# Kernel tuning notes

Measured on AMD Instinct MI355X. Metric: run time of the kernel, lower is better.

Reference implementation:

```python
import jax, jax.numpy as jnp
import numpy as np

N_OSC = 50
N_PER = 40
DT = 0.01
STEPS = 100
# one-link torque limb physical constants (reconstructed)
M_G_LC = 1.0   # m*g*lc gravity torque coefficient
B_DAMP = 0.1   # viscous damping
I_INERTIA = 1.0


def setup_inputs() -> dict:
    key = jax.random.key(0)
    ks = jax.random.split(key, 16)
    B = 8192
    x = jax.random.normal(ks[0], (B, 2), dtype=jnp.float32)
    fc1_w = jax.random.normal(ks[1], (128, 2), dtype=jnp.float32) * 0.5
    fc1_b = jax.random.normal(ks[2], (128,), dtype=jnp.float32) * 0.1
    fc2_w = jax.random.normal(ks[3], (128, 128), dtype=jnp.float32) * 0.08
    fc2_b = jax.random.normal(ks[4], (128,), dtype=jnp.float32) * 0.1
    fc3_w = jax.random.normal(ks[5], (N_OSC * 2, 128), dtype=jnp.float32) * 0.08
    fc3_b = jax.random.normal(ks[6], (N_OSC * 2,), dtype=jnp.float32) * 0.1
    fcd_w = jax.random.normal(ks[7], (1, 128), dtype=jnp.float32) * 0.001  # weight/100
    fcd_b = jnp.zeros((1,), dtype=jnp.float32)                            # bias*0
    enc = jax.random.normal(ks[8], (N_OSC, N_PER, 2), dtype=jnp.float32)
    obias = jax.random.normal(ks[9], (N_OSC, N_PER), dtype=jnp.float32)
    dec = jax.random.normal(ks[10], (N_OSC, 2, N_PER), dtype=jnp.float32) * 0.05
    fc4_w = jax.random.normal(ks[11], (1, N_OSC * N_PER), dtype=jnp.float32) * 1e-4  # weight/10000
    fc4_b = jnp.zeros((1,), dtype=jnp.float32)                                       # bias*0
    return {"x": x, "fc1_w": fc1_w, "fc1_b": fc1_b, "fc2_w": fc2_w, "fc2_b": fc2_b,
            "fc3_w": fc3_w, "fc3_b": fc3_b, "fcd_w": fcd_w, "fcd_b": fcd_b,
            "enc": enc, "obias": obias, "dec": dec, "fc4_w": fc4_w, "fc4_b": fc4_b}


def reference(x, fc1_w, fc1_b, fc2_w, fc2_b, fc3_w, fc3_b, fcd_w, fcd_b,
              enc, obias, dec, fc4_w, fc4_b):
    B = x.shape[0]
    h = jax.nn.relu(x @ fc1_w.T + fc1_b)            # (B,128)
    direct = h @ fcd_w.T + fcd_b                    # (B,1)
    h2 = jax.nn.relu(h @ fc2_w.T + fc2_b)           # (B,128)
    x3 = h2 @ fc3_w.T + fc3_b                       # (B, 2*N_OSC)
    o0 = x3.reshape(B, N_OSC, 2).transpose(1, 0, 2)  # (N_OSC,B,2), xi = x[:, 2j:2j+2]
    l0 = jnp.concatenate([x[:, :1], jnp.zeros((B, 1), dtype=x.dtype)], axis=1)  # (B,2)

    def step(carry, _):
        o, l = carry
        # NEF oscillator activities: relu(state @ encoders^T + bias), vectorized over oscillators
        a = jax.nn.relu(jnp.einsum('obd,ond->obn', o, enc) + obias[:, None, :])  # (N_OSC,B,N_PER)
        o_deriv = jnp.einsum('odn,obn->obd', dec, a)                             # (N_OSC,B,2)
        o = o + DT * o_deriv
        acts = a.transpose(1, 0, 2).reshape(B, N_OSC * N_PER)                    # (B,2000)
        torque = (acts @ fc4_w.T + fc4_b + direct)[:, 0]                         # (B,)
        theta, omega = l[:, 0], l[:, 1]
        alpha = (torque - M_G_LC * jnp.sin(theta) - B_DAMP * omega) / I_INERTIA
        l = l + DT * jnp.stack([omega, alpha], axis=1)
        return (o, l), (l, torque)

    _, (l_states, torques) = jax.lax.scan(step, (o0, l0), None, length=STEPS)
    return l_states, torques  # (STEPS,B,2), (STEPS,B)
```

## Files before the change

### kernel.cpp

```cpp
#include <hip/hip_runtime.h>

#define N_OSC 50
#define N_PER 40
#define DT 0.01f
#define STEPS 100
#define BATCH 8192

typedef float v2f __attribute__((ext_vector_type(2)));

static __device__ __forceinline__ v2f fma2(v2f a, v2f b, v2f c) {
    return __builtin_elementwise_fma(a, b, c);
}

#define WS_PC     0
#define WS_DIRECT 12288
#define WS_O0     20480
#define WS_TORQ   839680

__global__ __launch_bounds__(256) void prep_mlp_kernel(
    const float* __restrict__ x,
    const float* __restrict__ fc1_w, const float* __restrict__ fc1_b,
    const float* __restrict__ fc2_w, const float* __restrict__ fc2_b,
    const float* __restrict__ fc3_w, const float* __restrict__ fc3_b,
    const float* __restrict__ fcd_w, const float* __restrict__ fcd_b,
    const float* __restrict__ enc, const float* __restrict__ obias,
    const float* __restrict__ dec, const float* __restrict__ fc4_w,
    float* __restrict__ pc, float* __restrict__ torq,
    float* __restrict__ o0out, float* __restrict__ directout) {
    __shared__ float hs[16 * 132];
    __shared__ float h2s[16 * 132];
    int blk = blockIdx.x;
    int tid = threadIdx.x;

    if (blk < 800) {
        int idx = blk * 256 + tid;
        ((float4*)torq)[idx] = make_float4(0.f, 0.f, 0.f, 0.f);
        if (idx < N_OSC * N_PER) {
            int o = idx / N_PER, n = idx - o * N_PER;
            int c = n >> 1, h = n & 1;
            float* base = pc + o * 240;
            base[4 * c + h]           = enc[o * 80 + 2 * n + 0];
            base[4 * c + 2 + h]       = enc[o * 80 + 2 * n + 1];
            base[80 + 4 * c + h]      = dec[o * 80 + n];
            base[80 + 4 * c + 2 + h]  = dec[o * 80 + 40 + n];
            base[160 + 2 * c + h]     = fc4_w[o * 40 + n];
            base[200 + 2 * c + h]     = obias[o * 40 + n];
        }
        return;
    }

    int r = tid & 15;
    int jg = tid >> 4;
    int b0 = (blk - 800) * 16;

    for (int idx = tid; idx < 16 * 128; idx += 256) {
        int rr = idx >> 7, j = idx & 127;
        float x0 = x[(b0 + rr) * 2], x1 = x[(b0 + rr) * 2 + 1];
        float v = fmaf(x0, fc1_w[j * 2], fmaf(x1, fc1_w[j * 2 + 1], fc1_b[j]));
        hs[rr * 132 + j] = fmaxf(v, 0.f);
    }
    __syncthreads();

    if (tid < 16) {
        float s = fcd_b[0];
        #pragma unroll 8
        for (int k = 0; k < 128; k += 4) {
            float4 h4 = *(const float4*)&hs[tid * 132 + k];
            float4 w4 = *(const float4*)&fcd_w[k];
            s = fmaf(h4.x, w4.x, fmaf(h4.y, w4.y, fmaf(h4.z, w4.z, fmaf(h4.w, w4.w, s))));
        }
        directout[b0 + tid] = s;
    }

    for (int pass = 0; pass < 2; ++pass) {
        int j0 = jg * 8 + pass * 4;
        float a0 = fc2_b[j0], a1 = fc2_b[j0 + 1], a2 = fc2_b[j0 + 2], a3 = fc2_b[j0 + 3];
        const float* w0 = fc2_w + j0 * 128;
        const float* w1 = w0 + 128;
        const float* w2 = w0 + 256;
        const float* w3 = w0 + 384;
        #pragma unroll 8
        for (int k = 0; k < 128; k += 4) {
            float4 h4 = *(const float4*)&hs[r * 132 + k];
            float4 q0 = *(const float4*)&w0[k];
            float4 q1 = *(const float4*)&w1[k];
            float4 q2 = *(const float4*)&w2[k];
            float4 q3 = *(const float4*)&w3[k];
            a0 = fmaf(h4.x, q0.x, fmaf(h4.y, q0.y, fmaf(h4.z, q0.z, fmaf(h4.w, q0.w, a0))));
            a1 = fmaf(h4.x, q1.x, fmaf(h4.y, q1.y, fmaf(h4.z, q1.z, fmaf(h4.w, q1.w, a1))));
            a2 = fmaf(h4.x, q2.x, fmaf(h4.y, q2.y, fmaf(h4.z, q2.z, fmaf(h4.w, q2.w, a2))));
            a3 = fmaf(h4.x, q3.x, fmaf(h4.y, q3.y, fmaf(h4.z, q3.z, fmaf(h4.w, q3.w, a3))));
        }
        h2s[r * 132 + j0]     = fmaxf(a0, 0.f);
        h2s[r * 132 + j0 + 1] = fmaxf(a1, 0.f);
        h2s[r * 132 + j0 + 2] = fmaxf(a2, 0.f);
        h2s[r * 132 + j0 + 3] = fmaxf(a3, 0.f);
    }
    __syncthreads();

    for (int pass = 0; pass < 2; ++pass) {
        int j0 = pass * 64 + jg * 4;
        if (j0 >= 100) continue;
        float a0 = fc3_b[j0], a1 = fc3_b[j0 + 1], a2 = fc3_b[j0 + 2], a3 = fc3_b[j0 + 3];
        const float* w0 = fc3_w + j0 * 128;
        const float* w1 = w0 + 128;
        const float* w2 = w0 + 256;
        const float* w3 = w0 + 384;
        #pragma unroll 8
        for (int k = 0; k < 128; k += 4) {
            float4 h4 = *(const float4*)&h2s[r * 132 + k];
            float4 q0 = *(const float4*)&w0[k];
            float4 q1 = *(const float4*)&w1[k];
            float4 q2 = *(const float4*)&w2[k];
            float4 q3 = *(const float4*)&w3[k];
            a0 = fmaf(h4.x, q0.x, fmaf(h4.y, q0.y, fmaf(h4.z, q0.z, fmaf(h4.w, q0.w, a0))));
            a1 = fmaf(h4.x, q1.x, fmaf(h4.y, q1.y, fmaf(h4.z, q1.z, fmaf(h4.w, q1.w, a1))));
            a2 = fmaf(h4.x, q2.x, fmaf(h4.y, q2.y, fmaf(h4.z, q2.z, fmaf(h4.w, q2.w, a2))));
            a3 = fmaf(h4.x, q3.x, fmaf(h4.y, q3.y, fmaf(h4.z, q3.z, fmaf(h4.w, q3.w, a3))));
        }
        o0out[(j0)     * BATCH + b0 + r] = a0;
        o0out[(j0 + 1) * BATCH + b0 + r] = a1;
        o0out[(j0 + 2) * BATCH + b0 + r] = a2;
        o0out[(j0 + 3) * BATCH + b0 + r] = a3;
    }
}

__global__ __attribute__((amdgpu_waves_per_eu(4, 4))) __launch_bounds__(256)
void osc_kernel(const float* __restrict__ pc,
                const float* __restrict__ o0init,
                float* __restrict__ torq) {
    int tid = threadIdx.x;
    int w = __builtin_amdgcn_readfirstlane(tid >> 6);
    int lane = tid & 63;
    int W = blockIdx.x * 4 + w;
    int bg = W / N_OSC;
    int osc = W - bg * N_OSC;
    int ug = lane & 3;
    int b = bg * 16 + (lane >> 2);

    const float* __restrict__ base = pc + osc * 240;

    float4 E[5], Dv[5];
    v2f Wv[5], OB[5];
    #pragma unroll
    for (int i = 0; i < 5; ++i) {
        int c = ug * 5 + i;
        E[i]  = *(const float4*)(base + 4 * c);
        Dv[i] = *(const float4*)(base + 80 + 4 * c);
        Wv[i] = *(const v2f*)(base + 160 + 2 * c);
        OB[i] = *(const v2f*)(base + 200 + 2 * c);
    }
    #pragma unroll
    for (int i = 0; i < 5; ++i) {
        asm volatile("" : "+v"(E[i].x), "+v"(E[i].y), "+v"(E[i].z), "+v"(E[i].w));
        asm volatile("" : "+v"(Dv[i].x), "+v"(Dv[i].y), "+v"(Dv[i].z), "+v"(Dv[i].w));
        asm volatile("" : "+v"(Wv[i]), "+v"(OB[i]));
    }

    float s0 = o0init[(2 * osc) * BATCH + b];
    float s1 = o0init[(2 * osc + 1) * BATCH + b];
    float* tp = torq + b;

    for (int step = 0; step < STEPS; ++step) {
        v2f o0p = (v2f){s0, s0};
        v2f o1p = (v2f){s1, s1};
        v2f tq = (v2f){0.f, 0.f};
        v2f D0 = (v2f){0.f, 0.f};
        v2f D1 = (v2f){0.f, 0.f};
        #pragma unroll
        for (int i = 0; i < 5; ++i) {
            v2f e0 = (v2f){E[i].x, E[i].y};
            v2f e1 = (v2f){E[i].z, E[i].w};
            v2f a = fma2(o0p, e0, fma2(o1p, e1, OB[i]));
            a = __builtin_elementwise_max(a, (v2f){0.f, 0.f});
            tq = fma2(a, Wv[i], tq);
            D0 = fma2(a, (v2f){Dv[i].x, Dv[i].y}, D0);
            D1 = fma2(a, (v2f){Dv[i].z, Dv[i].w}, D1);
        }
        float v0 = D0.x + D0.y;
        float v1 = D1.x + D1.y;
        float vt = tq.x + tq.y;
        v0 += __shfl_xor(v0, 1, 64);  v0 += __shfl_xor(v0, 2, 64);
        v1 += __shfl_xor(v1, 1, 64);  v1 += __shfl_xor(v1, 2, 64);
        vt += __shfl_xor(vt, 1, 64);  vt += __shfl_xor(vt, 2, 64);
        s0 = fmaf(DT, v0, s0);
        s1 = fmaf(DT, v1, s1);
        if (ug == 0) atomicAdd(tp + step * BATCH, vt);
    }
}

__global__ __launch_bounds__(256) void pend_kernel(const float* __restrict__ x,
                                                   const float* __restrict__ torq,
                                                   const float* __restrict__ direct,
                                                   const float* __restrict__ fc4_b,
                                                   float* __restrict__ out) {
    int b = blockIdx.x * 256 + threadIdx.x;
    float theta = x[2 * b];
    float omega = 0.f;
    float base = direct[b] + fc4_b[0];
    float2* out_l = (float2*)out;
    float* out_t = out + STEPS * BATCH * 2;
    float pf[4];
    #pragma unroll
    for (int j = 0; j < 4; ++j) pf[j] = torq[j * BATCH + b];
    #pragma unroll 4
    for (int s = 0; s < STEPS; ++s) {
        float tq = base + pf[s & 3];
        if (s + 4 < STEPS) pf[s & 3] = torq[(s + 4) * BATCH + b];
        float alpha = tq - __sinf(theta) - 0.1f * omega;
        theta = fmaf(DT, omega, theta);
        omega = fmaf(DT, alpha, omega);
        out_l[s * BATCH + b] = make_float2(theta, omega);
        out_t[s * BATCH + b] = tq;
    }
}

extern "C" void kernel_launch(void* const* d_in, const int* in_sizes, int n_in,
                              void* d_out, int out_size, void* d_ws, size_t ws_size,
                              hipStream_t stream) {
    const float* x     = (const float*)d_in[0];
    const float* fc1_w = (const float*)d_in[1];
    const float* fc1_b = (const float*)d_in[2];
    const float* fc2_w = (const float*)d_in[3];
    const float* fc2_b = (const float*)d_in[4];
    const float* fc3_w = (const float*)d_in[5];
    const float* fc3_b = (const float*)d_in[6];
    const float* fcd_w = (const float*)d_in[7];
    const float* fcd_b = (const float*)d_in[8];
    const float* enc   = (const float*)d_in[9];
    const float* obias = (const float*)d_in[10];
    const float* dec   = (const float*)d_in[11];
    const float* fc4_w = (const float*)d_in[12];
    const float* fc4_b = (const float*)d_in[13];
    float* out = (float*)d_out;
    float* ws = (float*)d_ws;

    float* pc      = ws + WS_PC;
    float* direct  = ws + WS_DIRECT;
    float* o0      = ws + WS_O0;
    float* torq    = ws + WS_TORQ;

    hipLaunchKernelGGL(prep_mlp_kernel, dim3(800 + 512), dim3(256), 0, stream,
                       x, fc1_w, fc1_b, fc2_w, fc2_b, fc3_w, fc3_b,
                       fcd_w, fcd_b, enc, obias, dec, fc4_w,
                       pc, torq, o0, direct);
    hipLaunchKernelGGL(osc_kernel, dim3(25600 / 4), dim3(256), 0, stream,
                       pc, o0, torq);
    hipLaunchKernelGGL(pend_kernel, dim3(BATCH / 256), dim3(256), 0, stream,
                       x, torq, direct, fc4_b, out);
}
```

Before: 428.5 us.

## Hand-write oscillator loop in inline assembly and shrink pendulum blocks

Replaces the oscillator step loop with hand-written GCN assembly. It uses packed FMAs, DPP quad-permute reductions instead of shuffles, an exec-masked atomic add, and a fixed register allocation with the parameter loads issued inside the asm. The waves_per_eu attribute is removed. The pendulum kernel now launches 64-thread blocks, giving more workgroups across the CUs. The assembly hardcodes register numbers and instruction semantics, so it is fragile and stops the compiler from scheduling the loop.

```diff
diff --git a/kernel.cpp b/kernel.cpp
--- a/kernel.cpp
+++ b/kernel.cpp
@@ -5,12 +5,6 @@
 #define DT 0.01f
 #define STEPS 100
 #define BATCH 8192
-
-typedef float v2f __attribute__((ext_vector_type(2)));
-
-static __device__ __forceinline__ v2f fma2(v2f a, v2f b, v2f c) {
-    return __builtin_elementwise_fma(a, b, c);
-}
 
 #define WS_PC     0
 #define WS_DIRECT 12288
@@ -125,10 +119,9 @@
     }
 }
 
-__global__ __attribute__((amdgpu_waves_per_eu(4, 4))) __launch_bounds__(256)
-void osc_kernel(const float* __restrict__ pc,
-                const float* __restrict__ o0init,
-                float* __restrict__ torq) {
+__global__ __launch_bounds__(256) void osc_kernel(const float* __restrict__ pc,
+                                                  const float* __restrict__ o0init,
+                                                  float* __restrict__ torq) {
     int tid = threadIdx.x;
     int w = __builtin_amdgcn_readfirstlane(tid >> 6);
     int lane = tid & 63;
@@ -138,63 +131,132 @@
     int ug = lane & 3;
     int b = bg * 16 + (lane >> 2);
 
-    const float* __restrict__ base = pc + osc * 240;
-
-    float4 E[5], Dv[5];
-    v2f Wv[5], OB[5];
-    #pragma unroll
-    for (int i = 0; i < 5; ++i) {
-        int c = ug * 5 + i;
-        E[i]  = *(const float4*)(base + 4 * c);
-        Dv[i] = *(const float4*)(base + 80 + 4 * c);
-        Wv[i] = *(const v2f*)(base + 160 + 2 * c);
-        OB[i] = *(const v2f*)(base + 200 + 2 * c);
-    }
-    #pragma unroll
-    for (int i = 0; i < 5; ++i) {
-        asm volatile("" : "+v"(E[i].x), "+v"(E[i].y), "+v"(E[i].z), "+v"(E[i].w));
-        asm volatile("" : "+v"(Dv[i].x), "+v"(Dv[i].y), "+v"(Dv[i].z), "+v"(Dv[i].w));
-        asm volatile("" : "+v"(Wv[i]), "+v"(OB[i]));
-    }
+    const char* pcb = (const char*)(pc + osc * 240);
+    const char* addr1 = pcb + 16 * (ug * 5);
+    const char* addr2 = pcb + 8 * (ug * 5);
 
     float s0 = o0init[(2 * osc) * BATCH + b];
     float s1 = o0init[(2 * osc + 1) * BATCH + b];
-    float* tp = torq + b;
-
-    for (int step = 0; step < STEPS; ++step) {
-        v2f o0p = (v2f){s0, s0};
-        v2f o1p = (v2f){s1, s1};
-        v2f tq = (v2f){0.f, 0.f};
-        v2f D0 = (v2f){0.f, 0.f};
-        v2f D1 = (v2f){0.f, 0.f};
-        #pragma unroll
-        for (int i = 0; i < 5; ++i) {
-            v2f e0 = (v2f){E[i].x, E[i].y};
-            v2f e1 = (v2f){E[i].z, E[i].w};
-            v2f a = fma2(o0p, e0, fma2(o1p, e1, OB[i]));
-            a = __builtin_elementwise_max(a, (v2f){0.f, 0.f});
-            tq = fma2(a, Wv[i], tq);
-            D0 = fma2(a, (v2f){Dv[i].x, Dv[i].y}, D0);
-            D1 = fma2(a, (v2f){Dv[i].z, Dv[i].w}, D1);
-        }
-        float v0 = D0.x + D0.y;
-        float v1 = D1.x + D1.y;
-        float vt = tq.x + tq.y;
-        v0 += __shfl_xor(v0, 1, 64);  v0 += __shfl_xor(v0, 2, 64);
-        v1 += __shfl_xor(v1, 1, 64);  v1 += __shfl_xor(v1, 2, 64);
-        vt += __shfl_xor(vt, 1, 64);  vt += __shfl_xor(vt, 2, 64);
-        s0 = fmaf(DT, v0, s0);
-        s1 = fmaf(DT, v1, s1);
-        if (ug == 0) atomicAdd(tp + step * BATCH, vt);
-    }
+    unsigned long long ua = (unsigned long long)(torq + b);
+    unsigned int alo = (unsigned int)ua;
+    unsigned int ahi = (unsigned int)(ua >> 32);
+    unsigned long long mask = __ballot(ug == 0);
+    unsigned long long saved = 0;
+    int cnt = STEPS;
+    float dt = DT;
+
+    asm volatile(
+        "global_load_dwordx4 v[12:15], %[a1], off\n\t"
+        "global_load_dwordx4 v[16:19], %[a1], off offset:16\n\t"
+        "global_load_dwordx4 v[20:23], %[a1], off offset:32\n\t"
+        "global_load_dwordx4 v[24:27], %[a1], off offset:48\n\t"
+        "global_load_dwordx4 v[28:31], %[a1], off offset:64\n\t"
+        "global_load_dwordx4 v[32:35], %[a1], off offset:320\n\t"
+        "global_load_dwordx4 v[36:39], %[a1], off offset:336\n\t"
+        "global_load_dwordx4 v[40:43], %[a1], off offset:352\n\t"
+        "global_load_dwordx4 v[44:47], %[a1], off offset:368\n\t"
+        "global_load_dwordx4 v[48:51], %[a1], off offset:384\n\t"
+        "global_load_dwordx2 v[52:53], %[a2], off offset:640\n\t"
+        "global_load_dwordx2 v[54:55], %[a2], off offset:648\n\t"
+        "global_load_dwordx2 v[56:57], %[a2], off offset:656\n\t"
+        "global_load_dwordx2 v[58:59], %[a2], off offset:664\n\t"
+        "global_load_dwordx2 v[60:61], %[a2], off offset:672\n\t"
+        "global_load_dwordx2 v[62:63], %[a2], off offset:800\n\t"
+        "global_load_dwordx2 v[64:65], %[a2], off offset:808\n\t"
+        "global_load_dwordx2 v[66:67], %[a2], off offset:816\n\t"
+        "global_load_dwordx2 v[68:69], %[a2], off offset:824\n\t"
+        "global_load_dwordx2 v[70:71], %[a2], off offset:832\n\t"
+        "v_mov_b32 v72, 0\n\t"
+        "v_mov_b32 v73, 0\n\t"
+        "v_mov_b32 v74, %[alo]\n\t"
+        "v_mov_b32 v75, %[ahi]\n\t"
+        "s_waitcnt vmcnt(0)\n\t"
+        "Losc%=:\n\t"
+        "v_mov_b32 v0, %[s0]\n\t"
+        "v_mov_b32 v1, %[s0]\n\t"
+        "v_mov_b32 v2, %[s1]\n\t"
+        "v_mov_b32 v3, %[s1]\n\t"
+        "v_pk_fma_f32 v[4:5], v[2:3], v[14:15], v[62:63]\n\t"
+        "v_pk_fma_f32 v[4:5], v[0:1], v[12:13], v[4:5]\n\t"
+        "v_max_f32 v4, 0, v4\n\t"
+        "v_max_f32 v5, 0, v5\n\t"
+        "v_pk_mul_f32 v[6:7], v[4:5], v[52:53]\n\t"
+        "v_pk_mul_f32 v[8:9], v[4:5], v[32:33]\n\t"
+        "v_pk_mul_f32 v[10:11], v[4:5], v[34:35]\n\t"
+        "v_pk_fma_f32 v[4:5], v[2:3], v[18:19], v[64:65]\n\t"
+        "v_pk_fma_f32 v[4:5], v[0:1], v[16:17], v[4:5]\n\t"
+        "v_max_f32 v4, 0, v4\n\t"
+        "v_max_f32 v5, 0, v5\n\t"
+        "v_pk_fma_f32 v[6:7], v[4:5], v[54:55], v[6:7]\n\t"
+        "v_pk_fma_f32 v[8:9], v[4:5], v[36:37], v[8:9]\n\t"
+        "v_pk_fma_f32 v[10:11], v[4:5], v[38:39], v[10:11]\n\t"
+        "v_pk_fma_f32 v[4:5], v[2:3], v[22:23], v[66:67]\n\t"
+        "v_pk_fma_f32 v[4:5], v[0:1], v[20:21], v[4:5]\n\t"
+        "v_max_f32 v4, 0, v4\n\t"
+        "v_max_f32 v5, 0, v5\n\t"
+        "v_pk_fma_f32 v[6:7], v[4:5], v[56:57], v[6:7]\n\t"
+        "v_pk_fma_f32 v[8:9], v[4:5], v[40:41], v[8:9]\n\t"
+        "v_pk_fma_f32 v[10:11], v[4:5], v[42:43], v[10:11]\n\t"
+        "v_pk_fma_f32 v[4:5], v[2:3], v[26:27], v[68:69]\n\t"
+        "v_pk_fma_f32 v[4:5], v[0:1], v[24:25], v[4:5]\n\t"
+        "v_max_f32 v4, 0, v4\n\t"
+        "v_max_f32 v5, 0, v5\n\t"
+        "v_pk_fma_f32 v[6:7], v[4:5], v[58:59], v[6:7]\n\t"
+        "v_pk_fma_f32 v[8:9], v[4:5], v[44:45], v[8:9]\n\t"
+        "v_pk_fma_f32 v[10:11], v[4:5], v[46:47], v[10:11]\n\t"
+        "v_pk_fma_f32 v[4:5], v[2:3], v[30:31], v[70:71]\n\t"
+        "v_pk_fma_f32 v[4:5], v[0:1], v[28:29], v[4:5]\n\t"
+        "v_max_f32 v4, 0, v4\n\t"
+        "v_max_f32 v5, 0, v5\n\t"
+        "v_pk_fma_f32 v[6:7], v[4:5], v[60:61], v[6:7]\n\t"
+        "v_pk_fma_f32 v[8:9], v[4:5], v[48:49], v[8:9]\n\t"
+        "v_pk_fma_f32 v[10:11], v[4:5], v[50:51], v[10:11]\n\t"
+        "v_add_f32 v4, v8, v9\n\t"
+        "v_add_f32 v5, v10, v11\n\t"
+        "v_add_f32 v6, v6, v7\n\t"
+        "v_mov_b32_dpp v0, v4 quad_perm:[1,0,3,2] row_mask:0xf bank_mask:0xf\n\t"
+        "v_mov_b32_dpp v1, v5 quad_perm:[1,0,3,2] row_mask:0xf bank_mask:0xf\n\t"
+        "v_mov_b32_dpp v7, v6 quad_perm:[1,0,3,2] row_mask:0xf bank_mask:0xf\n\t"
+        "v_add_f32 v4, v4, v0\n\t"
+        "v_add_f32 v5, v5, v1\n\t"
+        "v_add_f32 v6, v6, v7\n\t"
+        "v_mov_b32_dpp v0, v4 quad_perm:[2,3,0,1] row_mask:0xf bank_mask:0xf\n\t"
+        "v_mov_b32_dpp v1, v5 quad_perm:[2,3,0,1] row_mask:0xf bank_mask:0xf\n\t"
+        "v_mov_b32_dpp v7, v6 quad_perm:[2,3,0,1] row_mask:0xf bank_mask:0xf\n\t"
+        "v_add_f32 v4, v4, v0\n\t"
+        "v_add_f32 v5, v5, v1\n\t"
+        "v_add_f32 v6, v6, v7\n\t"
+        "v_fmac_f32 %[s0], %[dt], v4\n\t"
+        "v_fmac_f32 %[s1], %[dt], v5\n\t"
+        "s_mov_b64 %[sv], exec\n\t"
+        "s_and_b64 exec, exec, %[mk]\n\t"
+        "global_atomic_add_f32 v[74:75], v6, off\n\t"
+        "s_mov_b64 exec, %[sv]\n\t"
+        "v_add_co_u32 v74, vcc, 0x8000, v74\n\t"
+        "v_addc_co_u32 v75, vcc, 0, v75, vcc\n\t"
+        "s_sub_u32 %[cnt], %[cnt], 1\n\t"
+        "s_cmp_lg_u32 %[cnt], 0\n\t"
+        "s_cbranch_scc1 Losc%=\n\t"
+        : [s0]"+v"(s0), [s1]"+v"(s1), [cnt]"+s"(cnt), [sv]"+s"(saved)
+        : [a1]"v"(addr1), [a2]"v"(addr2), [alo]"v"(alo), [ahi]"v"(ahi),
+          [dt]"v"(dt), [mk]"s"(mask)
+        : "memory", "vcc", "scc",
+          "v0","v1","v2","v3","v4","v5","v6","v7","v8","v9",
+          "v10","v11","v12","v13","v14","v15","v16","v17","v18","v19",
+          "v20","v21","v22","v23","v24","v25","v26","v27","v28","v29",
+          "v30","v31","v32","v33","v34","v35","v36","v37","v38","v39",
+          "v40","v41","v42","v43","v44","v45","v46","v47","v48","v49",
+          "v50","v51","v52","v53","v54","v55","v56","v57","v58","v59",
+          "v60","v61","v62","v63","v64","v65","v66","v67","v68","v69",
+          "v70","v71","v72","v73","v74","v75");
 }
 
-__global__ __launch_bounds__(256) void pend_kernel(const float* __restrict__ x,
-                                                   const float* __restrict__ torq,
-                                                   const float* __restrict__ direct,
-                                                   const float* __restrict__ fc4_b,
-                                                   float* __restrict__ out) {
-    int b = blockIdx.x * 256 + threadIdx.x;
+__global__ __launch_bounds__(64) void pend_kernel(const float* __restrict__ x,
+                                                  const float* __restrict__ torq,
+                                                  const float* __restrict__ direct,
+                                                  const float* __restrict__ fc4_b,
+                                                  float* __restrict__ out) {
+    int b = blockIdx.x * 64 + threadIdx.x;
     float theta = x[2 * b];
     float omega = 0.f;
     float base = direct[b] + fc4_b[0];
@@ -246,6 +308,6 @@
                        pc, torq, o0, direct);
     hipLaunchKernelGGL(osc_kernel, dim3(25600 / 4), dim3(256), 0, stream,
                        pc, o0, torq);
-    hipLaunchKernelGGL(pend_kernel, dim3(BATCH / 256), dim3(256), 0, stream,
+    hipLaunchKernelGGL(pend_kernel, dim3(BATCH / 64), dim3(64), 0, stream,
                        x, torq, direct, fc4_b, out);
 }
```

Result: slower. 442.2 us (+3.2%).
